# Optimization experiments

Measured on AMD Instinct MI355X. Metric: run time of the kernel, lower is better.

Reference implementation:

```python
import jax, jax.numpy as jnp
import numpy as np

H = 1024   # hidden size
E = 8      # num experts
B, S = 4, 2048


def setup_inputs() -> dict:
    key = jax.random.key(0)
    k1, k2, k3, k4 = jax.random.split(key, 4)
    x = jax.random.normal(k1, (B, S, H), dtype=jnp.float32)
    wg = jax.random.normal(k2, (H, E), dtype=jnp.float32) * 0.02      # gate weight
    W = jax.random.normal(k3, (E, H, H), dtype=jnp.float32) * 0.02    # expert Linear weights (out, in) per expert
    b = jax.random.normal(k4, (E, H), dtype=jnp.float32) * 0.02       # expert Linear biases
    return {"x": x, "wg": wg, "W": W, "b": b}


def reference(x, wg, W, b):
    Bb, Ss, Hh = x.shape
    Ee = wg.shape[1]
    T = Bb * Ss
    C = T // Ee  # capacity (capacity_factor = 1.0, top-1)

    xt = x.reshape(T, Hh)
    logits = xt @ wg                                   # [T, E]
    probs = jax.nn.softmax(logits, axis=-1)            # [T, E]
    idx = jnp.argmax(probs, axis=-1)                   # [T] top-1 expert
    mask = jax.nn.one_hot(idx, Ee, dtype=xt.dtype)     # [T, E]

    # position of each token within its expert's queue (0-based)
    locations = jnp.cumsum(mask, axis=0) - mask        # [T, E]
    # drop tokens over capacity
    mask = mask * (locations < C).astype(xt.dtype)
    gate = jnp.sum(probs * mask, axis=-1)              # [T] gate prob (0 if dropped)
    loc_s = jnp.sum(locations * mask, axis=-1).astype(jnp.int32)  # [T]
    loc_oh = jax.nn.one_hot(loc_s, C, dtype=xt.dtype)  # [T, C]

    dispatch = mask[:, :, None] * loc_oh[:, None, :]   # [T, E, C]
    combine = gate[:, None, None] * dispatch           # [T, E, C]

    # dispatch tokens -> per-expert buffers [E, C, H]
    exp_in = jnp.einsum('tec,th->ech', dispatch, xt)
    # per-expert Linear: y = x @ W_e^T + b_e
    exp_out = jnp.einsum('ech,efh->ecf', exp_in, W) + b[:, None, :]
    # combine back to tokens, scaled by gate prob
    out = jnp.einsum('tec,ecf->tf', combine, exp_out)  # [T, H]
    return out.reshape(Bb, Ss, Hh)
```

## Files before the change

### kernel.cpp

```cpp
#include <hip/hip_runtime.h>

#define H 1024
#define E 8
#define T 8192
#define CAP 1024

typedef __bf16 bf16x8 __attribute__((ext_vector_type(8)));
typedef float  f32x4  __attribute__((ext_vector_type(4)));
typedef unsigned short u16;

__device__ __forceinline__ u16 f2bf(float f) {
    union { float f; unsigned u; } v; v.f = f;
    unsigned r = v.u + 0x7FFFu + ((v.u >> 16) & 1u);
    return (u16)(r >> 16);
}

__device__ __forceinline__ unsigned cvt2bf(float lo, float hi) {
    unsigned r;
    asm("v_cvt_pk_bf16_f32 %0, %1, %2" : "=v"(r) : "v"(lo), "v"(hi));
    return r;
}

typedef __attribute__((address_space(1))) const void* gas_t;
typedef __attribute__((address_space(3))) void* las_t;
__device__ __forceinline__ void gld16(const void* g, void* l) {
    __builtin_amdgcn_global_load_lds((gas_t)g, (las_t)l, 16, 0, 0);
}

__global__ __launch_bounds__(256) void gate_kernel(
    const float* __restrict__ x, const float* __restrict__ wg,
    int* __restrict__ eid, float* __restrict__ gate, u16* __restrict__ xbf) {
    __shared__ float wgs[E][H];
    const int tid = threadIdx.x;

    {
        const int h0 = tid * 4;
        float4 lo[4], hi[4];
        #pragma unroll
        for (int r = 0; r < 4; ++r) {
            const float4* p = (const float4*)(wg + (size_t)(h0 + r) * E);
            lo[r] = p[0]; hi[r] = p[1];
        }
        #pragma unroll
        for (int e = 0; e < 4; ++e) {
            float4 v0 = make_float4(((const float*)&lo[0])[e], ((const float*)&lo[1])[e],
                                    ((const float*)&lo[2])[e], ((const float*)&lo[3])[e]);
            *(float4*)&wgs[e][h0] = v0;
            float4 v1 = make_float4(((const float*)&hi[0])[e], ((const float*)&hi[1])[e],
                                    ((const float*)&hi[2])[e], ((const float*)&hi[3])[e]);
            *(float4*)&wgs[e + 4][h0] = v1;
        }
    }
    __syncthreads();

    const int wv = tid >> 6, lane = tid & 63;
    const int tbase = blockIdx.x * 16 + wv * 4;
    const int h00 = lane * 4;

    float a[4][8];
    #pragma unroll
    for (int j = 0; j < 4; ++j)
        #pragma unroll
        for (int e = 0; e < 8; ++e) a[j][e] = 0.f;

    #pragma unroll
    for (int q = 0; q < 4; ++q) {
        const int h0 = q * 256 + h00;
        float4 xv[4];
        #pragma unroll
        for (int j = 0; j < 4; ++j)
            xv[j] = *(const float4*)(x + (size_t)(tbase + j) * H + h0);
        #pragma unroll
        for (int j = 0; j < 4; ++j) {
            ushort4 o;
            o.x = f2bf(xv[j].x); o.y = f2bf(xv[j].y);
            o.z = f2bf(xv[j].z); o.w = f2bf(xv[j].w);
            *(ushort4*)(xbf + (size_t)(tbase + j) * H + h0) = o;
        }
        #pragma unroll
        for (int e = 0; e < 8; ++e) {
            const float4 w4 = *(const float4*)&wgs[e][h0];
            #pragma unroll
            for (int j = 0; j < 4; ++j)
                a[j][e] += xv[j].x * w4.x + xv[j].y * w4.y
                         + xv[j].z * w4.z + xv[j].w * w4.w;
        }
    }

    const bool b0 = lane & 1, b1 = lane & 2, b2 = lane & 4;
    const int elane = ((lane & 1) << 2) | (lane & 2) | ((lane >> 2) & 1);

    #pragma unroll
    for (int j = 0; j < 4; ++j) {
        float* A = a[j];
        #pragma unroll
        for (int k = 0; k < 4; ++k) {
            float t = b0 ? A[k] : A[k + 4];
            t = __shfl_xor(t, 1);
            A[k] = (b0 ? A[k + 4] : A[k]) + t;
        }
        #pragma unroll
        for (int k = 0; k < 2; ++k) {
            float t = b1 ? A[k] : A[k + 2];
            t = __shfl_xor(t, 2);
            A[k] = (b1 ? A[k + 2] : A[k]) + t;
        }
        {
            float t = b2 ? A[0] : A[1];
            t = __shfl_xor(t, 4);
            A[0] = (b2 ? A[1] : A[0]) + t;
        }
        float v = A[0];
        v += __shfl_xor(v, 8); v += __shfl_xor(v, 16); v += __shfl_xor(v, 32);
        float m = v; int mi = elane;
        #pragma unroll
        for (int off = 1; off <= 4; off <<= 1) {
            float om = __shfl_xor(m, off);
            int   oi = __shfl_xor(mi, off);
            if (om > m || (om == m && oi < mi)) { m = om; mi = oi; }
        }
        float s = expf(v - m);
        s += __shfl_xor(s, 1); s += __shfl_xor(s, 2); s += __shfl_xor(s, 4);
        if (lane == 0) {
            eid[tbase + j]  = mi;
            gate[tbase + j] = 1.0f / s;
        }
    }
}

#define SCAN_T 1024
#define STPT 8
__global__ __launch_bounds__(1024) void scan_kernel(
    const int* __restrict__ eid, float* __restrict__ gate,
    int* __restrict__ perm) {
    __shared__ int cnt[SCAN_T][E];
    __shared__ int part[E][32];
    const int tid = threadIdx.x;

    for (int i = tid; i < E * CAP; i += SCAN_T) perm[i] = -1;

    const int t0 = tid * STPT;
    int ei[STPT];
    #pragma unroll
    for (int i = 0; i < STPT; ++i) ei[i] = eid[t0 + i];

    int c[E];
    #pragma unroll
    for (int e = 0; e < E; ++e) c[e] = 0;
    #pragma unroll
    for (int i = 0; i < STPT; ++i)
        #pragma unroll
        for (int e = 0; e < E; ++e) c[e] += (ei[i] == e);
    #pragma unroll
    for (int e = 0; e < E; ++e) cnt[tid][e] = c[e];
    __syncthreads();

    if (tid < 256) {
        const int e = tid >> 5, g = tid & 31;
        int s = 0;
        for (int i = g * 32; i < g * 32 + 32; ++i) s += cnt[i][e];
        part[e][g] = s;
    }
    __syncthreads();
    if (tid < E) {
        int run = 0;
        #pragma unroll
        for (int g = 0; g < 32; ++g) { int v = part[tid][g]; part[tid][g] = run; run += v; }
    }
    __syncthreads();
    if (tid < 256) {
        const int e = tid >> 5, g = tid & 31;
        int run = part[e][g];
        for (int i = g * 32; i < g * 32 + 32; ++i) { int v = cnt[i][e]; cnt[i][e] = run; run += v; }
    }
    __syncthreads();

    #pragma unroll
    for (int e = 0; e < E; ++e) c[e] = cnt[tid][e];
    #pragma unroll
    for (int i = 0; i < STPT; ++i) {
        const int t = t0 + i, e0 = ei[i];
        int pos = 0;
        #pragma unroll
        for (int k = 0; k < E; ++k) if (e0 == k) pos = c[k]++;
        if (pos < CAP) perm[e0 * CAP + pos] = t;
        else gate[t] = 0.f;
    }
}

__global__ __launch_bounds__(512, 4) void moe_gemm_bf(
    const u16* __restrict__ xbf, const float* __restrict__ W,
    const float* __restrict__ bias, const int* __restrict__ perm,
    const float* __restrict__ gate, float* __restrict__ out) {
    __shared__ __align__(16) u16 As[2][128 * 64];
    __shared__ __align__(16) u16 Bs[2][128 * 64];
    __shared__ int   perm_s[128];
    __shared__ float gate_s[128];

    const int tid = threadIdx.x;
    const int bid = blockIdx.x;

    if (bid < 64) {
        const int t = bid * 128 + (tid >> 2);
        if (gate[t] == 0.f) {
            const int part = tid & 3;
            float4 z = make_float4(0.f, 0.f, 0.f, 0.f);
            float4* o = (float4*)(out + (size_t)t * H + part * 256);
            #pragma unroll
            for (int i = 0; i < 64; ++i) o[i] = z;
        }
        return;
    }

    const int idx = bid - 64;
    const int fb = idx >> 6;
    const int mb = (idx >> 3) & 7;
    const int e  = idx & 7;

    if (tid < 128) {
        const int t = perm[e * CAP + mb * 128 + tid];
        perm_s[tid] = t;
        gate_s[tid] = (t >= 0) ? gate[t] : 0.f;
    }
    __syncthreads();

    const int lane = tid & 63;
    const int wv = tid >> 6;
    const int wm = wv >> 2;
    const int wn = wv & 3;
    const int l16 = lane & 15, quad = lane >> 4;

    const int rl  = lane >> 3;
    const int cch = lane & 7;
    const int gch = cch ^ rl;
    const u16*   ga[2];
    const float* gb[2];
    #pragma unroll
    for (int q = 0; q < 2; ++q) {
        const int r = wv * 16 + q * 8 + rl;
        const int tA = perm_s[r];
        const int tok = tA >= 0 ? tA : 0;
        ga[q] = xbf + (size_t)tok * H + gch * 8;
        gb[q] = W + (size_t)e * H * H + (size_t)(fb * 128 + r) * H + gch * 8;
    }

    f32x4 acc[4][2] = {};

    uint4 pw[4];
    #pragma unroll
    for (int hb = 0; hb < 2; ++hb)
        #pragma unroll
        for (int q = 0; q < 2; ++q) {
            const float4* p = (const float4*)(gb[q] + hb * 64);
            const float4 v0 = p[0], v1 = p[1];
            uint4 v;
            v.x = cvt2bf(v0.x, v0.y); v.y = cvt2bf(v0.z, v0.w);
            v.z = cvt2bf(v1.x, v1.y); v.w = cvt2bf(v1.z, v1.w);
            pw[hb * 2 + q] = v;
        }

    for (int kt = 0; kt < H / 128; ++kt) {
        __syncthreads();
        #pragma unroll
        for (int hb = 0; hb < 2; ++hb)
            #pragma unroll
            for (int q = 0; q < 2; ++q) {
                u16* la = &As[hb][(wv * 16 + q * 8) * 64 + lane * 8];
                gld16(ga[q] + hb * 64, la);
            }
        #pragma unroll
        for (int hb = 0; hb < 2; ++hb)
            #pragma unroll
            for (int q = 0; q < 2; ++q)
                *(uint4*)&Bs[hb][(wv * 16 + q * 8 + rl) * 64 + cch * 8] = pw[hb * 2 + q];
        #pragma unroll
        for (int q = 0; q < 2; ++q) { ga[q] += 128; gb[q] += 128; }
        __syncthreads();

        if (kt < H / 128 - 1) {
            #pragma unroll
            for (int hb = 0; hb < 2; ++hb)
                #pragma unroll
                for (int q = 0; q < 2; ++q) {
                    const float4* p = (const float4*)(gb[q] + hb * 64);
                    const float4 v0 = p[0], v1 = p[1];
                    uint4 v;
                    v.x = cvt2bf(v0.x, v0.y); v.y = cvt2bf(v0.z, v0.w);
                    v.z = cvt2bf(v1.x, v1.y); v.w = cvt2bf(v1.z, v1.w);
                    pw[hb * 2 + q] = v;
                }
        }

        #pragma unroll
        for (int hb = 0; hb < 2; ++hb)
            #pragma unroll
            for (int s = 0; s < 2; ++s) {
                bf16x8 af[4], bfr[2];
                const int cc = (s * 4 + quad) ^ (l16 & 7);
                #pragma unroll
                for (int i = 0; i < 4; ++i)
                    af[i] = *(const bf16x8*)&As[hb][(wm * 64 + i * 16 + l16) * 64 + cc * 8];
                #pragma unroll
                for (int i = 0; i < 2; ++i)
                    bfr[i] = *(const bf16x8*)&Bs[hb][(wn * 32 + i * 16 + l16) * 64 + cc * 8];
                #pragma unroll
                for (int mi = 0; mi < 4; ++mi)
                    #pragma unroll
                    for (int ni = 0; ni < 2; ++ni)
                        acc[mi][ni] = __builtin_amdgcn_mfma_f32_16x16x32_bf16(
                            af[mi], bfr[ni], acc[mi][ni], 0, 0, 0);
            }
    }

    float bv[2];
    #pragma unroll
    for (int ni = 0; ni < 2; ++ni)
        bv[ni] = bias[e * H + fb * 128 + wn * 32 + ni * 16 + l16];

    #pragma unroll
    for (int mi = 0; mi < 4; ++mi) {
        #pragma unroll
        for (int r = 0; r < 4; ++r) {
            const int rowl = wm * 64 + mi * 16 + quad * 4 + r;
            const int t = perm_s[rowl];
            if (t < 0) continue;
            const float g = gate_s[rowl];
            float* orow = out + (size_t)t * H + fb * 128 + wn * 32;
            #pragma unroll
            for (int ni = 0; ni < 2; ++ni)
                orow[ni * 16 + l16] = g * (acc[mi][ni][r] + bv[ni]);
        }
    }
}

extern "C" void kernel_launch(void* const* d_in, const int* in_sizes, int n_in,
                              void* d_out, int out_size, void* d_ws, size_t ws_size,
                              hipStream_t stream) {
    const float* x    = (const float*)d_in[0];
    const float* wg   = (const float*)d_in[1];
    const float* W    = (const float*)d_in[2];
    const float* bias = (const float*)d_in[3];
    float* out = (float*)d_out;

    int*   eid  = (int*)d_ws;
    float* gate = (float*)((char*)d_ws + (size_t)T * 4);
    int*   perm = (int*)((char*)d_ws + (size_t)T * 8);
    u16*   xbf  = (u16*)((char*)d_ws + (size_t)T * 12);

    gate_kernel<<<T / 16, 256, 0, stream>>>(x, wg, eid, gate, xbf);
    scan_kernel<<<1, SCAN_T, 0, stream>>>(eid, gate, perm);
    moe_gemm_bf<<<64 + 512, 512, 0, stream>>>(xbf, W, bias, perm, gate, out);
}
```

Before: 159.4 us.

## Double-buffer expert GEMM K-loop in 64-wide steps and drop gate LDS staging

The expert GEMM main loop now ping-pongs between two LDS halves at K=64 granularity. It issues the global loads for the next A and B tiles before the MFMAs on the current tile, and converts and stores B to LDS afterwards, with one barrier per step instead of two. This is meant to overlap global latency with compute, at the cost of more iterations and barriers in total. Separately, the gate kernel no longer transposes wg into shared memory; each thread reads its wg rows directly from global memory (cache), removing the LDS staging and its block sync.

```diff
diff --git a/kernel.cpp b/kernel.cpp
--- a/kernel.cpp
+++ b/kernel.cpp
@@ -30,29 +30,7 @@
 __global__ __launch_bounds__(256) void gate_kernel(
     const float* __restrict__ x, const float* __restrict__ wg,
     int* __restrict__ eid, float* __restrict__ gate, u16* __restrict__ xbf) {
-    __shared__ float wgs[E][H];
     const int tid = threadIdx.x;
-
-    {
-        const int h0 = tid * 4;
-        float4 lo[4], hi[4];
-        #pragma unroll
-        for (int r = 0; r < 4; ++r) {
-            const float4* p = (const float4*)(wg + (size_t)(h0 + r) * E);
-            lo[r] = p[0]; hi[r] = p[1];
-        }
-        #pragma unroll
-        for (int e = 0; e < 4; ++e) {
-            float4 v0 = make_float4(((const float*)&lo[0])[e], ((const float*)&lo[1])[e],
-                                    ((const float*)&lo[2])[e], ((const float*)&lo[3])[e]);
-            *(float4*)&wgs[e][h0] = v0;
-            float4 v1 = make_float4(((const float*)&hi[0])[e], ((const float*)&hi[1])[e],
-                                    ((const float*)&hi[2])[e], ((const float*)&hi[3])[e]);
-            *(float4*)&wgs[e + 4][h0] = v1;
-        }
-    }
-    __syncthreads();
-
     const int wv = tid >> 6, lane = tid & 63;
     const int tbase = blockIdx.x * 16 + wv * 4;
     const int h00 = lane * 4;
@@ -77,14 +55,20 @@
             o.z = f2bf(xv[j].z); o.w = f2bf(xv[j].w);
             *(ushort4*)(xbf + (size_t)(tbase + j) * H + h0) = o;
         }
-        #pragma unroll
-        for (int e = 0; e < 8; ++e) {
-            const float4 w4 = *(const float4*)&wgs[e][h0];
+        float wr[4][8];
+        #pragma unroll
+        for (int r = 0; r < 4; ++r) {
+            const float4* p = (const float4*)(wg + (size_t)(h0 + r) * E);
+            float4 lo = p[0], hi = p[1];
+            wr[r][0] = lo.x; wr[r][1] = lo.y; wr[r][2] = lo.z; wr[r][3] = lo.w;
+            wr[r][4] = hi.x; wr[r][5] = hi.y; wr[r][6] = hi.z; wr[r][7] = hi.w;
+        }
+        #pragma unroll
+        for (int e = 0; e < 8; ++e)
             #pragma unroll
             for (int j = 0; j < 4; ++j)
-                a[j][e] += xv[j].x * w4.x + xv[j].y * w4.y
-                         + xv[j].z * w4.z + xv[j].w * w4.w;
-        }
+                a[j][e] += xv[j].x * wr[0][e] + xv[j].y * wr[1][e]
+                         + xv[j].z * wr[2][e] + xv[j].w * wr[3][e];
     }
 
     const bool b0 = lane & 1, b1 = lane & 2, b2 = lane & 4;
@@ -246,71 +230,79 @@
 
     f32x4 acc[4][2] = {};
 
-    uint4 pw[4];
-    #pragma unroll
-    for (int hb = 0; hb < 2; ++hb)
+    {
+        float4 nb[2][2];
         #pragma unroll
         for (int q = 0; q < 2; ++q) {
-            const float4* p = (const float4*)(gb[q] + hb * 64);
-            const float4 v0 = p[0], v1 = p[1];
+            const float4* p = (const float4*)gb[q];
+            nb[q][0] = p[0]; nb[q][1] = p[1];
+        }
+        #pragma unroll
+        for (int q = 0; q < 2; ++q)
+            gld16(ga[q], &As[0][(wv * 16 + q * 8) * 64 + lane * 8]);
+        #pragma unroll
+        for (int q = 0; q < 2; ++q) {
             uint4 v;
-            v.x = cvt2bf(v0.x, v0.y); v.y = cvt2bf(v0.z, v0.w);
-            v.z = cvt2bf(v1.x, v1.y); v.w = cvt2bf(v1.z, v1.w);
-            pw[hb * 2 + q] = v;
-        }
-
-    for (int kt = 0; kt < H / 128; ++kt) {
-        __syncthreads();
-        #pragma unroll
-        for (int hb = 0; hb < 2; ++hb)
-            #pragma unroll
-            for (int q = 0; q < 2; ++q) {
-                u16* la = &As[hb][(wv * 16 + q * 8) * 64 + lane * 8];
-                gld16(ga[q] + hb * 64, la);
-            }
-        #pragma unroll
-        for (int hb = 0; hb < 2; ++hb)
-            #pragma unroll
-            for (int q = 0; q < 2; ++q)
-                *(uint4*)&Bs[hb][(wv * 16 + q * 8 + rl) * 64 + cch * 8] = pw[hb * 2 + q];
-        #pragma unroll
-        for (int q = 0; q < 2; ++q) { ga[q] += 128; gb[q] += 128; }
-        __syncthreads();
-
-        if (kt < H / 128 - 1) {
-            #pragma unroll
-            for (int hb = 0; hb < 2; ++hb)
-                #pragma unroll
-                for (int q = 0; q < 2; ++q) {
-                    const float4* p = (const float4*)(gb[q] + hb * 64);
-                    const float4 v0 = p[0], v1 = p[1];
-                    uint4 v;
-                    v.x = cvt2bf(v0.x, v0.y); v.y = cvt2bf(v0.z, v0.w);
-                    v.z = cvt2bf(v1.x, v1.y); v.w = cvt2bf(v1.z, v1.w);
-                    pw[hb * 2 + q] = v;
-                }
-        }
-
-        #pragma unroll
-        for (int hb = 0; hb < 2; ++hb)
-            #pragma unroll
-            for (int s = 0; s < 2; ++s) {
-                bf16x8 af[4], bfr[2];
-                const int cc = (s * 4 + quad) ^ (l16 & 7);
-                #pragma unroll
-                for (int i = 0; i < 4; ++i)
-                    af[i] = *(const bf16x8*)&As[hb][(wm * 64 + i * 16 + l16) * 64 + cc * 8];
-                #pragma unroll
-                for (int i = 0; i < 2; ++i)
-                    bfr[i] = *(const bf16x8*)&Bs[hb][(wn * 32 + i * 16 + l16) * 64 + cc * 8];
-                #pragma unroll
-                for (int mi = 0; mi < 4; ++mi)
-                    #pragma unroll
-                    for (int ni = 0; ni < 2; ++ni)
-                        acc[mi][ni] = __builtin_amdgcn_mfma_f32_16x16x32_bf16(
-                            af[mi], bfr[ni], acc[mi][ni], 0, 0, 0);
-            }
-    }
+            v.x = cvt2bf(nb[q][0].x, nb[q][0].y); v.y = cvt2bf(nb[q][0].z, nb[q][0].w);
+            v.z = cvt2bf(nb[q][1].x, nb[q][1].y); v.w = cvt2bf(nb[q][1].z, nb[q][1].w);
+            *(uint4*)&Bs[0][(wv * 16 + q * 8 + rl) * 64 + cch * 8] = v;
+        }
+        #pragma unroll
+        for (int q = 0; q < 2; ++q) { ga[q] += 64; gb[q] += 64; }
+    }
+    __syncthreads();
+
+#define STEP(CUR, NXT, PF)                                                    \
+    {                                                                         \
+        float4 nb[2][2];                                                      \
+        if (PF) {                                                             \
+            _Pragma("unroll")                                                 \
+            for (int q = 0; q < 2; ++q) {                                     \
+                const float4* p = (const float4*)gb[q];                       \
+                nb[q][0] = p[0]; nb[q][1] = p[1];                             \
+            }                                                                 \
+            _Pragma("unroll")                                                 \
+            for (int q = 0; q < 2; ++q)                                       \
+                gld16(ga[q], &As[NXT][(wv * 16 + q * 8) * 64 + lane * 8]);    \
+        }                                                                     \
+        _Pragma("unroll")                                                     \
+        for (int s = 0; s < 2; ++s) {                                         \
+            bf16x8 af[4], bfr[2];                                             \
+            const int cc = (s * 4 + quad) ^ (l16 & 7);                        \
+            _Pragma("unroll")                                                 \
+            for (int i = 0; i < 4; ++i)                                       \
+                af[i] = *(const bf16x8*)&As[CUR][(wm * 64 + i * 16 + l16) * 64 + cc * 8]; \
+            _Pragma("unroll")                                                 \
+            for (int i = 0; i < 2; ++i)                                       \
+                bfr[i] = *(const bf16x8*)&Bs[CUR][(wn * 32 + i * 16 + l16) * 64 + cc * 8]; \
+            _Pragma("unroll")                                                 \
+            for (int mi = 0; mi < 4; ++mi)                                    \
+                _Pragma("unroll")                                             \
+                for (int ni = 0; ni < 2; ++ni)                                \
+                    acc[mi][ni] = __builtin_amdgcn_mfma_f32_16x16x32_bf16(    \
+                        af[mi], bfr[ni], acc[mi][ni], 0, 0, 0);               \
+        }                                                                     \
+        if (PF) {                                                             \
+            _Pragma("unroll")                                                 \
+            for (int q = 0; q < 2; ++q) {                                     \
+                uint4 v;                                                      \
+                v.x = cvt2bf(nb[q][0].x, nb[q][0].y); v.y = cvt2bf(nb[q][0].z, nb[q][0].w); \
+                v.z = cvt2bf(nb[q][1].x, nb[q][1].y); v.w = cvt2bf(nb[q][1].z, nb[q][1].w); \
+                *(uint4*)&Bs[NXT][(wv * 16 + q * 8 + rl) * 64 + cch * 8] = v; \
+            }                                                                 \
+            _Pragma("unroll")                                                 \
+            for (int q = 0; q < 2; ++q) { ga[q] += 64; gb[q] += 64; }         \
+        }                                                                     \
+        __syncthreads();                                                      \
+    }
+
+    for (int kt2 = 0; kt2 < 7; ++kt2) {
+        STEP(0, 1, true)
+        STEP(1, 0, true)
+    }
+    STEP(0, 1, true)
+    STEP(1, 0, false)
+#undef STEP
 
     float bv[2];
     #pragma unroll
```

Measured after the change: 165.3 us. 1.04x slower.
